# Performance work log

Measured on AMD Instinct MI355X. Metric: run time of the kernel, lower is better.

## Reference

```python
import jax, jax.numpy as jnp
import numpy as np

N_NODES = 100000
N_EDGES = 1600000
IN_C, HID_C, OUT_C = 128, 64, 64


def setup_inputs() -> dict:
    key = jax.random.key(0)
    ks = jax.random.split(key, 9)
    x = jax.random.normal(ks[0], (N_NODES, IN_C), dtype=jnp.float32)
    src = jax.random.randint(ks[1], (N_EDGES,), 0, N_NODES, dtype=jnp.int64)
    dst = jax.random.randint(ks[2], (N_EDGES,), 0, N_NODES, dtype=jnp.int64)
    # Glorot-ish init for linear weights
    W1 = jax.random.normal(ks[3], (IN_C, HID_C), dtype=jnp.float32) / np.sqrt(IN_C)
    b1 = jnp.zeros((HID_C,), dtype=jnp.float32)
    W2 = jax.random.normal(ks[4], (HID_C, HID_C), dtype=jnp.float32) / np.sqrt(HID_C)
    b2 = jnp.zeros((HID_C,), dtype=jnp.float32)
    W3 = jax.random.normal(ks[5], (HID_C, OUT_C), dtype=jnp.float32) / np.sqrt(HID_C)
    b3 = jnp.zeros((OUT_C,), dtype=jnp.float32)
    return {"x": x, "src": src, "dst": dst,
            "W1": W1, "b1": b1, "W2": W2, "b2": b2, "W3": W3, "b3": b3}


def _gcn_conv(x, src, dst, W, b):
    # GCNConv(normalize=False): out = A @ (x W) + b  (unweighted sum aggregation)
    h = x @ W                          # [N, d_out] dense transform first (d_out small)
    msg = h[src]                       # gather per edge: [E, d_out]
    agg = jax.ops.segment_sum(msg, dst, num_segments=N_NODES)  # scatter-add
    return agg + b


def reference(x, src, dst, W1, b1, W2, b2, W3, b3):
    # layer 1..num_layers-1: conv -> activation -> dropout(eval: no-op)
    h = jax.nn.relu(_gcn_conv(x, src, dst, W1, b1))
    h = jax.nn.relu(_gcn_conv(h, src, dst, W2, b2))
    # last layer: conv -> activation
    out = jax.nn.relu(_gcn_conv(h, src, dst, W3, b3))
    return out
```

## Files before the change

### kernel.cpp

```cpp
#include <hip/hip_runtime.h>

#define N_NODES_C 100000
#define N_EDGES_C 1600000
#define NCHUNK 256
#define CHH (N_EDGES_C / NCHUNK)
#define NPART 128
#define CHP (N_EDGES_C / NPART)
#define BUCK_SH 7
#define BUCK_NODES 128
#define NB_BUCK 782

typedef short short8 __attribute__((ext_vector_type(8)));
typedef float f32x4 __attribute__((ext_vector_type(4)));
typedef float f32x2 __attribute__((ext_vector_type(2)));

__device__ __forceinline__ short f2bf(float f) {
  unsigned u = __builtin_bit_cast(unsigned, f);
  unsigned r = (u + 0x7FFFu + ((u >> 16) & 1u)) >> 16;
  return (short)r;
}

__device__ __forceinline__ unsigned char f32_to_fp8_hw(float x) {
  return (unsigned char)(__builtin_amdgcn_cvt_pk_fp8_f32(x, x, 0, false) & 0xFF);
}

template <int K>
__device__ __forceinline__ void gemm64_body(
    int gblock, const float* __restrict__ in_, const float* __restrict__ W,
    unsigned char* __restrict__ out_, int n_rows) {
  constexpr int KS = K / 32;
  int wave = threadIdx.x >> 6;
  int lane = threadIdx.x & 63;
  int row0 = (gblock * 4 + wave) * 16;
  if (row0 >= n_rows) return;

  int lrow = lane & 15;
  int lk = (lane >> 4) * 8;

  short8 bfrag[KS][4];
#pragma unroll
  for (int ks = 0; ks < KS; ++ks)
#pragma unroll
    for (int nt = 0; nt < 4; ++nt) {
      short8 b;
#pragma unroll
      for (int j = 0; j < 8; ++j)
        b[j] = f2bf(W[(size_t)(ks * 32 + lk + j) * 64 + nt * 16 + lrow]);
      bfrag[ks][nt] = b;
    }

  int row = row0 + lrow;
  f32x4 acc[4] = {};
#pragma unroll
  for (int ks = 0; ks < KS; ++ks) {
    short8 a;
    const float* ip = in_ + (size_t)row * K + ks * 32 + lk;
    f32x4 v0 = *(const f32x4*)(ip);
    f32x4 v1 = *(const f32x4*)(ip + 4);
#pragma unroll
    for (int j = 0; j < 4; ++j) {
      a[j] = f2bf(v0[j]);
      a[4 + j] = f2bf(v1[j]);
    }
#pragma unroll
    for (int nt = 0; nt < 4; ++nt)
      acc[nt] = __builtin_amdgcn_mfma_f32_16x16x32_bf16(a, bfrag[ks][nt],
                                                        acc[nt], 0, 0, 0);
  }

  int crow = row0 + (lane >> 4) * 4;
#pragma unroll
  for (int nt = 0; nt < 4; ++nt) {
    int ocol = nt * 16 + lrow;
#pragma unroll
    for (int r = 0; r < 4; ++r)
      out_[(size_t)(crow + r) * 64 + ocol] = f32_to_fp8_hw(acc[nt][r]);
  }
}

__global__ __launch_bounds__(256) void hist_gemm1_kernel(
    const int* __restrict__ dst, int* __restrict__ countsT,
    const float* __restrict__ x, const float* __restrict__ W1,
    unsigned char* __restrict__ hA, int n_rows) {
  __shared__ int lhist[NB_BUCK];
  int b = (int)blockIdx.x;
  if (b >= NCHUNK) {
    gemm64_body<128>(b - NCHUNK, x, W1, hA, n_rows);
    return;
  }
  for (int i = threadIdx.x; i < NB_BUCK; i += 256) lhist[i] = 0;
  __syncthreads();
  int beg = b * CHH, end = beg + CHH;
  for (int i = beg + (int)threadIdx.x; i < end; i += 256)
    atomicAdd(&lhist[((unsigned)dst[i]) >> BUCK_SH], 1);
  __syncthreads();
  for (int bb = threadIdx.x; bb < NB_BUCK; bb += 256)
    countsT[bb * NCHUNK + b] = lhist[bb];
}

__global__ __launch_bounds__(256) void scan_buckets_kernel(
    int* __restrict__ countsT, int* __restrict__ btot) {
  int b = blockIdx.x * 4 + (threadIdx.x >> 6);
  int lane = threadIdx.x & 63;
  if (b >= NB_BUCK) return;
  int4 v = *(const int4*)(countsT + b * NCHUNK + lane * 4);
  int s = v.x + v.y + v.z + v.w;
  int incl = s;
#pragma unroll
  for (int d = 1; d < 64; d <<= 1) {
    int t = __shfl_up(incl, d, 64);
    if (lane >= d) incl += t;
  }
  int excl = incl - s;
  int4 o;
  o.x = excl;
  o.y = excl + v.x;
  o.z = o.y + v.y;
  o.w = o.z + v.z;
  *(int4*)(countsT + b * NCHUNK + lane * 4) = o;
  if (lane == 63) btot[b] = incl;
}

__global__ __launch_bounds__(1024) void scan_btot_kernel(
    const int* __restrict__ btot, int* __restrict__ bstart) {
  __shared__ int lds[1024];
  int t = threadIdx.x;
  int v = (t < NB_BUCK) ? btot[t] : 0;
  lds[t] = v;
  __syncthreads();
  for (int off = 1; off < 1024; off <<= 1) {
    int tv = (t >= off) ? lds[t - off] : 0;
    __syncthreads();
    lds[t] += tv;
    __syncthreads();
  }
  if (t < NB_BUCK) bstart[t] = lds[t] - v;
  if (t == NB_BUCK - 1) bstart[NB_BUCK] = lds[t];
}

__global__ __launch_bounds__(1024) void partition_kernel(
    const int* __restrict__ src, const int* __restrict__ dst,
    const int* __restrict__ offs ,
    const int* __restrict__ bstart, unsigned* __restrict__ packed) {
  __shared__ int cur[NB_BUCK];
  int b = (int)blockIdx.x;
  for (int bb = threadIdx.x; bb < NB_BUCK; bb += 1024)
    cur[bb] = bstart[bb] + offs[bb * NCHUNK + 2 * b];
  __syncthreads();
  int beg = b * CHP, end = beg + CHP;
  for (int i = beg + (int)threadIdx.x; i < end; i += 1024) {
    int d = dst[i];
    int s = src[i];
    int bb = ((unsigned)d) >> BUCK_SH;
    int pos = atomicAdd(&cur[bb], 1);
    packed[pos] = ((unsigned)(d & (BUCK_NODES - 1)) << 17) | (unsigned)s;
  }
}

__global__ __launch_bounds__(256) void sort_bucket_kernel(
    const unsigned* __restrict__ packed, const int* __restrict__ bstart,
    int* __restrict__ col, int* __restrict__ row_ptr, int n_nodes,
    int n_edges) {
  __shared__ int lhist[BUCK_NODES];
  __shared__ int lcur[BUCK_NODES];
  __shared__ int wsum0;
  int b = (int)blockIdx.x;
  int beg = bstart[b], end = bstart[b + 1];
  int t = (int)threadIdx.x;

  if (t < BUCK_NODES) lhist[t] = 0;
  __syncthreads();
  for (int e = beg + t; e < end; e += 256)
    atomicAdd(&lhist[packed[e] >> 17], 1);
  __syncthreads();

  int v = 0, incl = 0;
  if (t < BUCK_NODES) {
    v = lhist[t];
    incl = v;
#pragma unroll
    for (int d = 1; d < 64; d <<= 1) {
      int u = __shfl_up(incl, d, 64);
      if ((t & 63) >= d) incl += u;
    }
  }
  if (t == 63) wsum0 = incl;
  __syncthreads();
  if (t >= 64 && t < BUCK_NODES) incl += wsum0;
  if (t < BUCK_NODES) {
    int excl = incl - v;
    lcur[t] = excl;
    int node = b * BUCK_NODES + t;
    if (node < n_nodes) row_ptr[node] = beg + excl;
  }
  if (b == NB_BUCK - 1 && t == 0) row_ptr[n_nodes] = n_edges;
  __syncthreads();

  for (int e = beg + t; e < end; e += 256) {
    unsigned pe = packed[e];
    int ld = (int)(pe >> 17);
    int pos = beg + atomicAdd(&lcur[ld], 1);
    col[pos] = (int)(pe & 0x1FFFFu);
  }
}

__device__ __forceinline__ void agg_node(
    const unsigned char* __restrict__ h, const int* __restrict__ col, int beg,
    int end, int slot, int q, float& s0, float& s1, float& s2, float& s3) {
  s0 = s1 = s2 = s3 = 0.f;
  float t0 = 0.f, t1 = 0.f, t2 = 0.f, t3 = 0.f;
  int e = beg + slot;
  for (; e + 12 < end; e += 16) {
    int sa = col[e];
    int sb = col[e + 4];
    int sc = col[e + 8];
    int sd = col[e + 12];
    int ua = *(const int*)(h + (size_t)sa * 64 + q * 4);
    int ub = *(const int*)(h + (size_t)sb * 64 + q * 4);
    int uc = *(const int*)(h + (size_t)sc * 64 + q * 4);
    int ud = *(const int*)(h + (size_t)sd * 64 + q * 4);
    f32x2 al = __builtin_amdgcn_cvt_pk_f32_fp8(ua, false);
    f32x2 ah = __builtin_amdgcn_cvt_pk_f32_fp8(ua, true);
    f32x2 bl = __builtin_amdgcn_cvt_pk_f32_fp8(ub, false);
    f32x2 bh = __builtin_amdgcn_cvt_pk_f32_fp8(ub, true);
    f32x2 cl = __builtin_amdgcn_cvt_pk_f32_fp8(uc, false);
    f32x2 ch = __builtin_amdgcn_cvt_pk_f32_fp8(uc, true);
    f32x2 dl = __builtin_amdgcn_cvt_pk_f32_fp8(ud, false);
    f32x2 dh = __builtin_amdgcn_cvt_pk_f32_fp8(ud, true);
    s0 += al[0] + bl[0];
    s1 += al[1] + bl[1];
    s2 += ah[0] + bh[0];
    s3 += ah[1] + bh[1];
    t0 += cl[0] + dl[0];
    t1 += cl[1] + dl[1];
    t2 += ch[0] + dh[0];
    t3 += ch[1] + dh[1];
  }
  for (; e < end; e += 4) {
    int sa = col[e];
    int ua = *(const int*)(h + (size_t)sa * 64 + q * 4);
    f32x2 al = __builtin_amdgcn_cvt_pk_f32_fp8(ua, false);
    f32x2 ah = __builtin_amdgcn_cvt_pk_f32_fp8(ua, true);
    s0 += al[0];
    s1 += al[1];
    s2 += ah[0];
    s3 += ah[1];
  }
  s0 += t0;
  s1 += t1;
  s2 += t2;
  s3 += t3;
  s0 += __shfl_xor(s0, 16);
  s1 += __shfl_xor(s1, 16);
  s2 += __shfl_xor(s2, 16);
  s3 += __shfl_xor(s3, 16);
  s0 += __shfl_xor(s0, 32);
  s1 += __shfl_xor(s1, 32);
  s2 += __shfl_xor(s2, 32);
  s3 += __shfl_xor(s3, 32);
}

__global__ __launch_bounds__(256) void agg_gemm_kernel(
    const unsigned char* __restrict__ h, const int* __restrict__ row_ptr,
    const int* __restrict__ col, const float* __restrict__ bias,
    const float* __restrict__ W, unsigned char* __restrict__ outg,
    int n_nodes) {
  __shared__ float rowbuf[16][68];
  int wid = threadIdx.x >> 6;
  int lane = threadIdx.x & 63;
  int slot = lane >> 4;
  int q = lane & 15;
  int nbase = blockIdx.x * 16;

#pragma unroll
  for (int n = 0; n < 4; ++n) {
    int ln = wid * 4 + n;
    int node = nbase + ln;
    float s0, s1, s2, s3;
    agg_node(h, col, row_ptr[node], row_ptr[node + 1], slot, q, s0, s1, s2, s3);
    if (lane < 16) {
      f32x4 r;
      r[0] = fmaxf(s0 + bias[q * 4 + 0], 0.f);
      r[1] = fmaxf(s1 + bias[q * 4 + 1], 0.f);
      r[2] = fmaxf(s2 + bias[q * 4 + 2], 0.f);
      r[3] = fmaxf(s3 + bias[q * 4 + 3], 0.f);
      *(f32x4*)&rowbuf[ln][q * 4] = r;
    }
  }
  __syncthreads();

  int lrow = lane & 15;
  int lk = (lane >> 4) * 8;
  f32x4 acc = {};
#pragma unroll
  for (int ks = 0; ks < 2; ++ks) {
    short8 a, bv;
#pragma unroll
    for (int j = 0; j < 8; ++j) a[j] = f2bf(rowbuf[lrow][ks * 32 + lk + j]);
#pragma unroll
    for (int j = 0; j < 8; ++j)
      bv[j] = f2bf(W[(size_t)(ks * 32 + lk + j) * 64 + wid * 16 + lrow]);
    acc = __builtin_amdgcn_mfma_f32_16x16x32_bf16(a, bv, acc, 0, 0, 0);
  }
  int crow = (lane >> 4) * 4;
#pragma unroll
  for (int r = 0; r < 4; ++r)
    outg[(size_t)(nbase + crow + r) * 64 + wid * 16 + lrow] =
        f32_to_fp8_hw(acc[r]);
}

__global__ __launch_bounds__(256) void agg_final_kernel(
    const unsigned char* __restrict__ h, const int* __restrict__ row_ptr,
    const int* __restrict__ col, const float* __restrict__ bias,
    float* __restrict__ out, int n_nodes) {
  int node = blockIdx.x * 4 + (threadIdx.x >> 6);
  if (node >= n_nodes) return;
  int lane = threadIdx.x & 63;
  int slot = lane >> 4;
  int q = lane & 15;
  float s0, s1, s2, s3;
  agg_node(h, col, row_ptr[node], row_ptr[node + 1], slot, q, s0, s1, s2, s3);
  if (lane < 16) {
    float4 v;
    v.x = fmaxf(s0 + bias[q * 4 + 0], 0.f);
    v.y = fmaxf(s1 + bias[q * 4 + 1], 0.f);
    v.z = fmaxf(s2 + bias[q * 4 + 2], 0.f);
    v.w = fmaxf(s3 + bias[q * 4 + 3], 0.f);
    ((float4*)out)[(size_t)node * 16 + q] = v;
  }
}

extern "C" void kernel_launch(void* const* d_in, const int* in_sizes, int n_in,
                              void* d_out, int out_size, void* d_ws,
                              size_t ws_size, hipStream_t stream) {
  const float* x = (const float*)d_in[0];
  const int* src = (const int*)d_in[1];
  const int* dst = (const int*)d_in[2];
  const float* W1 = (const float*)d_in[3];
  const float* b1 = (const float*)d_in[4];
  const float* W2 = (const float*)d_in[5];
  const float* b2 = (const float*)d_in[6];
  const float* W3 = (const float*)d_in[7];
  const float* b3 = (const float*)d_in[8];
  float* out = (float*)d_out;

  const int N = N_NODES_C;
  const int E = N_EDGES_C;

  char* ws = (char*)d_ws;
  int* countsT = (int*)(ws + 0);
  int* btot = (int*)(ws + (1u << 20));
  int* bstart = (int*)(ws + (1u << 20) + (16u << 10));
  int* row_ptr = (int*)(ws + (2u << 20));
  unsigned* packed = (unsigned*)(ws + (3u << 20));
  int* col = (int*)(ws + (10u << 20));
  unsigned char* hA = (unsigned char*)(ws + (17u << 20));
  unsigned char* hB = (unsigned char*)(ws + (24u << 20));

  const int gemm_grid = (N + 63) / 64;
  const int k1_grid = (NB_BUCK + 3) / 4;
  const int aggg_grid = N / 16;
  const int aggf_grid = (N + 3) / 4;

  hist_gemm1_kernel<<<NCHUNK + gemm_grid, 256, 0, stream>>>(dst, countsT, x,
                                                            W1, hA, N);
  scan_buckets_kernel<<<k1_grid, 256, 0, stream>>>(countsT, btot);
  scan_btot_kernel<<<1, 1024, 0, stream>>>(btot, bstart);
  partition_kernel<<<NPART, 1024, 0, stream>>>(src, dst, countsT, bstart,
                                               packed);
  sort_bucket_kernel<<<NB_BUCK, 256, 0, stream>>>(packed, bstart, col, row_ptr,
                                                  N, E);

  agg_gemm_kernel<<<aggg_grid, 256, 0, stream>>>(hA, row_ptr, col, b1, W2, hB,
                                                 N);
  agg_gemm_kernel<<<aggg_grid, 256, 0, stream>>>(hB, row_ptr, col, b2, W3, hA,
                                                 N);
  agg_final_kernel<<<aggf_grid, 256, 0, stream>>>(hA, row_ptr, col, b3, out, N);
}
```

Before: 204.8 us.

## Use 16-byte fp8 row loads with two nodes per wavefront in aggregation

The neighbor aggregation now has each lane load 16 fp8 bytes (uint4) instead of 4 bytes, so a 64-byte row is covered by 4 lanes and each half-wavefront handles one node with 8 edge slots. This is meant to cut the number of memory instructions per gathered row and raise edge-level parallelism for average-degree-16 nodes. The final kernel packs 8 nodes per block accordingly. In exchange each lane holds 16 accumulators plus 16 temporaries, which raises register pressure, and the cross-slot shuffle reduction now takes three steps.

```diff
diff --git a/kernel.cpp b/kernel.cpp
--- a/kernel.cpp
+++ b/kernel.cpp
@@ -204,60 +204,60 @@
   }
 }
 
-__device__ __forceinline__ void agg_node(
+__device__ __forceinline__ void agg_node_dual(
     const unsigned char* __restrict__ h, const int* __restrict__ col, int beg,
-    int end, int slot, int q, float& s0, float& s1, float& s2, float& s3) {
-  s0 = s1 = s2 = s3 = 0.f;
-  float t0 = 0.f, t1 = 0.f, t2 = 0.f, t3 = 0.f;
+    int end, int slot, int q, f32x2* acc) {
+  f32x2 tacc[8];
+#pragma unroll
+  for (int i = 0; i < 8; ++i) {
+    acc[i] = 0.f;
+    tacc[i] = 0.f;
+  }
   int e = beg + slot;
-  for (; e + 12 < end; e += 16) {
+  for (; e + 8 < end; e += 16) {
     int sa = col[e];
-    int sb = col[e + 4];
-    int sc = col[e + 8];
-    int sd = col[e + 12];
-    int ua = *(const int*)(h + (size_t)sa * 64 + q * 4);
-    int ub = *(const int*)(h + (size_t)sb * 64 + q * 4);
-    int uc = *(const int*)(h + (size_t)sc * 64 + q * 4);
-    int ud = *(const int*)(h + (size_t)sd * 64 + q * 4);
-    f32x2 al = __builtin_amdgcn_cvt_pk_f32_fp8(ua, false);
-    f32x2 ah = __builtin_amdgcn_cvt_pk_f32_fp8(ua, true);
-    f32x2 bl = __builtin_amdgcn_cvt_pk_f32_fp8(ub, false);
-    f32x2 bh = __builtin_amdgcn_cvt_pk_f32_fp8(ub, true);
-    f32x2 cl = __builtin_amdgcn_cvt_pk_f32_fp8(uc, false);
-    f32x2 ch = __builtin_amdgcn_cvt_pk_f32_fp8(uc, true);
-    f32x2 dl = __builtin_amdgcn_cvt_pk_f32_fp8(ud, false);
-    f32x2 dh = __builtin_amdgcn_cvt_pk_f32_fp8(ud, true);
-    s0 += al[0] + bl[0];
-    s1 += al[1] + bl[1];
-    s2 += ah[0] + bh[0];
-    s3 += ah[1] + bh[1];
-    t0 += cl[0] + dl[0];
-    t1 += cl[1] + dl[1];
-    t2 += ch[0] + dh[0];
-    t3 += ch[1] + dh[1];
-  }
-  for (; e < end; e += 4) {
+    int sb = col[e + 8];
+    uint4 ua = *(const uint4*)(h + (size_t)sa * 64 + q * 16);
+    uint4 ub = *(const uint4*)(h + (size_t)sb * 64 + q * 16);
+    acc[0] += __builtin_amdgcn_cvt_pk_f32_fp8((int)ua.x, false);
+    acc[1] += __builtin_amdgcn_cvt_pk_f32_fp8((int)ua.x, true);
+    acc[2] += __builtin_amdgcn_cvt_pk_f32_fp8((int)ua.y, false);
+    acc[3] += __builtin_amdgcn_cvt_pk_f32_fp8((int)ua.y, true);
+    acc[4] += __builtin_amdgcn_cvt_pk_f32_fp8((int)ua.z, false);
+    acc[5] += __builtin_amdgcn_cvt_pk_f32_fp8((int)ua.z, true);
+    acc[6] += __builtin_amdgcn_cvt_pk_f32_fp8((int)ua.w, false);
+    acc[7] += __builtin_amdgcn_cvt_pk_f32_fp8((int)ua.w, true);
+    tacc[0] += __builtin_amdgcn_cvt_pk_f32_fp8((int)ub.x, false);
+    tacc[1] += __builtin_amdgcn_cvt_pk_f32_fp8((int)ub.x, true);
+    tacc[2] += __builtin_amdgcn_cvt_pk_f32_fp8((int)ub.y, false);
+    tacc[3] += __builtin_amdgcn_cvt_pk_f32_fp8((int)ub.y, true);
+    tacc[4] += __builtin_amdgcn_cvt_pk_f32_fp8((int)ub.z, false);
+    tacc[5] += __builtin_amdgcn_cvt_pk_f32_fp8((int)ub.z, true);
+    tacc[6] += __builtin_amdgcn_cvt_pk_f32_fp8((int)ub.w, false);
+    tacc[7] += __builtin_amdgcn_cvt_pk_f32_fp8((int)ub.w, true);
+  }
+  for (; e < end; e += 8) {
     int sa = col[e];
-    int ua = *(const int*)(h + (size_t)sa * 64 + q * 4);
-    f32x2 al = __builtin_amdgcn_cvt_pk_f32_fp8(ua, false);
-    f32x2 ah = __builtin_amdgcn_cvt_pk_f32_fp8(ua, true);
-    s0 += al[0];
-    s1 += al[1];
-    s2 += ah[0];
-    s3 += ah[1];
-  }
-  s0 += t0;
-  s1 += t1;
-  s2 += t2;
-  s3 += t3;
-  s0 += __shfl_xor(s0, 16);
-  s1 += __shfl_xor(s1, 16);
-  s2 += __shfl_xor(s2, 16);
-  s3 += __shfl_xor(s3, 16);
-  s0 += __shfl_xor(s0, 32);
-  s1 += __shfl_xor(s1, 32);
-  s2 += __shfl_xor(s2, 32);
-  s3 += __shfl_xor(s3, 32);
+    uint4 ua = *(const uint4*)(h + (size_t)sa * 64 + q * 16);
+    acc[0] += __builtin_amdgcn_cvt_pk_f32_fp8((int)ua.x, false);
+    acc[1] += __builtin_amdgcn_cvt_pk_f32_fp8((int)ua.x, true);
+    acc[2] += __builtin_amdgcn_cvt_pk_f32_fp8((int)ua.y, false);
+    acc[3] += __builtin_amdgcn_cvt_pk_f32_fp8((int)ua.y, true);
+    acc[4] += __builtin_amdgcn_cvt_pk_f32_fp8((int)ua.z, false);
+    acc[5] += __builtin_amdgcn_cvt_pk_f32_fp8((int)ua.z, true);
+    acc[6] += __builtin_amdgcn_cvt_pk_f32_fp8((int)ua.w, false);
+    acc[7] += __builtin_amdgcn_cvt_pk_f32_fp8((int)ua.w, true);
+  }
+#pragma unroll
+  for (int i = 0; i < 8; ++i) acc[i] += tacc[i];
+#pragma unroll
+  for (int d = 4; d <= 16; d <<= 1) {
+#pragma unroll
+    for (int i = 0; i < 8; ++i) {
+      acc[i][0] += __shfl_xor(acc[i][0], d);
+      acc[i][1] += __shfl_xor(acc[i][1], d);
+    }
+  }
 }
 
 __global__ __launch_bounds__(256) void agg_gemm_kernel(
@@ -268,30 +268,34 @@
   __shared__ float rowbuf[16][68];
   int wid = threadIdx.x >> 6;
   int lane = threadIdx.x & 63;
-  int slot = lane >> 4;
-  int q = lane & 15;
+  int half = lane >> 5;
+  int slot = (lane >> 2) & 7;
+  int q = lane & 3;
   int nbase = blockIdx.x * 16;
 
 #pragma unroll
-  for (int n = 0; n < 4; ++n) {
-    int ln = wid * 4 + n;
+  for (int n = 0; n < 2; ++n) {
+    int ln = wid * 4 + n * 2 + half;
     int node = nbase + ln;
-    float s0, s1, s2, s3;
-    agg_node(h, col, row_ptr[node], row_ptr[node + 1], slot, q, s0, s1, s2, s3);
-    if (lane < 16) {
-      f32x4 r;
-      r[0] = fmaxf(s0 + bias[q * 4 + 0], 0.f);
-      r[1] = fmaxf(s1 + bias[q * 4 + 1], 0.f);
-      r[2] = fmaxf(s2 + bias[q * 4 + 2], 0.f);
-      r[3] = fmaxf(s3 + bias[q * 4 + 3], 0.f);
-      *(f32x4*)&rowbuf[ln][q * 4] = r;
+    f32x2 acc[8];
+    agg_node_dual(h, col, row_ptr[node], row_ptr[node + 1], slot, q, acc);
+    if ((lane & 31) < 4) {
+#pragma unroll
+      for (int wv = 0; wv < 4; ++wv) {
+        f32x4 r;
+        r[0] = fmaxf(acc[2 * wv][0] + bias[q * 16 + wv * 4 + 0], 0.f);
+        r[1] = fmaxf(acc[2 * wv][1] + bias[q * 16 + wv * 4 + 1], 0.f);
+        r[2] = fmaxf(acc[2 * wv + 1][0] + bias[q * 16 + wv * 4 + 2], 0.f);
+        r[3] = fmaxf(acc[2 * wv + 1][1] + bias[q * 16 + wv * 4 + 3], 0.f);
+        *(f32x4*)&rowbuf[ln][q * 16 + wv * 4] = r;
+      }
     }
   }
   __syncthreads();
 
   int lrow = lane & 15;
   int lk = (lane >> 4) * 8;
-  f32x4 acc = {};
+  f32x4 acc2 = {};
 #pragma unroll
   for (int ks = 0; ks < 2; ++ks) {
     short8 a, bv;
@@ -300,33 +304,42 @@
 #pragma unroll
     for (int j = 0; j < 8; ++j)
       bv[j] = f2bf(W[(size_t)(ks * 32 + lk + j) * 64 + wid * 16 + lrow]);
-    acc = __builtin_amdgcn_mfma_f32_16x16x32_bf16(a, bv, acc, 0, 0, 0);
+    acc2 = __builtin_amdgcn_mfma_f32_16x16x32_bf16(a, bv, acc2, 0, 0, 0);
   }
   int crow = (lane >> 4) * 4;
 #pragma unroll
   for (int r = 0; r < 4; ++r)
     outg[(size_t)(nbase + crow + r) * 64 + wid * 16 + lrow] =
-        f32_to_fp8_hw(acc[r]);
+        f32_to_fp8_hw(acc2[r]);
 }
 
 __global__ __launch_bounds__(256) void agg_final_kernel(
     const unsigned char* __restrict__ h, const int* __restrict__ row_ptr,
     const int* __restrict__ col, const float* __restrict__ bias,
     float* __restrict__ out, int n_nodes) {
-  int node = blockIdx.x * 4 + (threadIdx.x >> 6);
-  if (node >= n_nodes) return;
+  int wid = threadIdx.x >> 6;
   int lane = threadIdx.x & 63;
-  int slot = lane >> 4;
-  int q = lane & 15;
-  float s0, s1, s2, s3;
-  agg_node(h, col, row_ptr[node], row_ptr[node + 1], slot, q, s0, s1, s2, s3);
-  if (lane < 16) {
-    float4 v;
-    v.x = fmaxf(s0 + bias[q * 4 + 0], 0.f);
-    v.y = fmaxf(s1 + bias[q * 4 + 1], 0.f);
-    v.z = fmaxf(s2 + bias[q * 4 + 2], 0.f);
-    v.w = fmaxf(s3 + bias[q * 4 + 3], 0.f);
-    ((float4*)out)[(size_t)node * 16 + q] = v;
+  int half = lane >> 5;
+  int slot = (lane >> 2) & 7;
+  int q = lane & 3;
+  int node = blockIdx.x * 8 + wid * 2 + half;
+  int beg = 0, end = 0;
+  if (node < n_nodes) {
+    beg = row_ptr[node];
+    end = row_ptr[node + 1];
+  }
+  f32x2 acc[8];
+  agg_node_dual(h, col, beg, end, slot, q, acc);
+  if (node < n_nodes && (lane & 31) < 4) {
+#pragma unroll
+    for (int wv = 0; wv < 4; ++wv) {
+      f32x4 r;
+      r[0] = fmaxf(acc[2 * wv][0] + bias[q * 16 + wv * 4 + 0], 0.f);
+      r[1] = fmaxf(acc[2 * wv][1] + bias[q * 16 + wv * 4 + 1], 0.f);
+      r[2] = fmaxf(acc[2 * wv + 1][0] + bias[q * 16 + wv * 4 + 2], 0.f);
+      r[3] = fmaxf(acc[2 * wv + 1][1] + bias[q * 16 + wv * 4 + 3], 0.f);
+      *((f32x4*)out + (size_t)node * 16 + q * 4 + wv) = r;
+    }
   }
 }
 
@@ -360,7 +373,7 @@
   const int gemm_grid = (N + 63) / 64;
   const int k1_grid = (NB_BUCK + 3) / 4;
   const int aggg_grid = N / 16;
-  const int aggf_grid = (N + 3) / 4;
+  const int aggf_grid = (N + 7) / 8;
 
   hist_gemm1_kernel<<<NCHUNK + gemm_grid, 256, 0, stream>>>(dst, countsT, x,
                                                             W1, hA, N);
```

After: 176.3 us. 1.16x faster.
